# Kernel tuning notes

Measured on AMD Instinct MI355X. Metric: run time of the kernel, lower is better.

Reference implementation:

```python
import jax, jax.numpy as jnp
import numpy as np

TOP_K = 2
NORM_TOPK_PROB = True


def setup_inputs() -> dict:
    key = jax.random.key(0)
    k1, k2 = jax.random.split(key)
    hidden_states = jax.random.normal(k1, (4, 4096, 2048), dtype=jnp.float32)
    # gate weight [n_routed_experts, hidden_size], kaiming-uniform-like scale
    weight = jax.random.normal(k2, (64, 2048), dtype=jnp.float32) * 0.02
    return {"hidden_states": hidden_states, "weight": weight}


def reference(hidden_states, weight):
    bsz, seq_len, h = hidden_states.shape
    x = hidden_states.reshape(-1, h)                      # [T, H]
    logits = jnp.einsum("th,eh->te", x, weight)           # [T, E]
    scores = jax.nn.softmax(logits, axis=-1)              # [T, E]
    topk_weight, topk_idx = jax.lax.top_k(scores, TOP_K)  # [T, K] each
    if TOP_K > 1 and NORM_TOPK_PROB:
        topk_weight = topk_weight / (topk_weight.sum(axis=-1, keepdims=True) + 1e-20)
    return (topk_idx.reshape(bsz, seq_len, -1), topk_weight.reshape(bsz, seq_len, -1))
```

## Files before the change

kernel.cpp:

```cpp
#include <hip/hip_runtime.h>
#include <math.h>

#define H    2048
#define NE   64
#define TOKB 32
#define KC   64
#define NCH  (H / KC)
#define TAU  4.0e-3f
#define NEGF (-3.0e38f)

typedef __bf16 bf16x8 __attribute__((ext_vector_type(8)));
typedef float  f32x16 __attribute__((ext_vector_type(16)));

#define MFMA(a, b, c) __builtin_amdgcn_mfma_f32_32x32x16_bf16((a), (b), (c), 0, 0, 0)
#define LD4(p) (*reinterpret_cast<const float4*>(p))

__device__ __forceinline__ void cvt8(const float4 a, const float4 b,
                                     bf16x8& hi, bf16x8& lo) {
    const float v0 = a.x, v1 = a.y, v2 = a.z, v3 = a.w;
    const float v4 = b.x, v5 = b.y, v6 = b.z, v7 = b.w;
    hi[0] = (__bf16)v0; lo[0] = (__bf16)(v0 - (float)hi[0]);
    hi[1] = (__bf16)v1; lo[1] = (__bf16)(v1 - (float)hi[1]);
    hi[2] = (__bf16)v2; lo[2] = (__bf16)(v2 - (float)hi[2]);
    hi[3] = (__bf16)v3; lo[3] = (__bf16)(v3 - (float)hi[3]);
    hi[4] = (__bf16)v4; lo[4] = (__bf16)(v4 - (float)hi[4]);
    hi[5] = (__bf16)v5; lo[5] = (__bf16)(v5 - (float)hi[5]);
    hi[6] = (__bf16)v6; lo[6] = (__bf16)(v6 - (float)hi[6]);
    hi[7] = (__bf16)v7; lo[7] = (__bf16)(v7 - (float)hi[7]);
}

__device__ __forceinline__ void gll16(const float* g, float* l) {
    __builtin_amdgcn_global_load_lds(
        (const __attribute__((address_space(1))) void*)g,
        (__attribute__((address_space(3))) void*)l, 16, 0, 0);
}

__global__ void zero_wl(int* __restrict__ wl) {
    if (threadIdx.x == 0) wl[0] = 0;
}

__global__ __launch_bounds__(256) void moe_gate_mfma(
    const float* __restrict__ x,
    const float* __restrict__ w,
    float* __restrict__ out,
    int woff,
    int* __restrict__ wl, int wlcap)
{
    __shared__ float lds[2][6144];

    const int tid  = threadIdx.x;
    const int lane = tid & 63;
    const int kq   = tid >> 6;
    const int lo5  = lane & 31;
    const int hi5  = lane >> 5;
    const int t0   = blockIdx.x * TOKB;

    const float* sbase[6];
    #pragma unroll
    for (int s = 0; s < 6; ++s) {
        const int idx = kq * 1536 + s * 256 + lane * 4;
        const int tr  = (idx & 4095) >> 6;
        const int sl  = (lane & 15) ^ (tr & 15);
        sbase[s] = (idx < 4096)
            ? (w + (size_t)tr * H + sl * 4)
            : (x + (size_t)(t0 + tr) * H + sl * 4);
    }

    f32x16 acc0, acc1;
    #pragma unroll
    for (int i = 0; i < 16; ++i) { acc0[i] = 0.f; acc1[i] = 0.f; }

    #pragma unroll
    for (int s = 0; s < 6; ++s)
        gll16(sbase[s], &lds[0][kq * 1536 + s * 256]);
    __syncthreads();

    const int s0 = kq * 4 + hi5 * 2;

    for (int c = 0; c < NCH; ++c) {
        const int cur = c & 1;
        if (c + 1 < NCH) {
            const int kc = (c + 1) * KC;
            #pragma unroll
            for (int s = 0; s < 6; ++s)
                gll16(sbase[s] + kc, &lds[cur ^ 1][kq * 1536 + s * 256]);
        }

        const float* buf = lds[cur];
        const int rb  = lo5;
        const int ra0 = lo5, ra1 = 32 + lo5;

        const float4 b1  = LD4(&buf[4096 + rb * 64 + ((s0     ^ (rb  & 15)) << 2)]);
        const float4 b2  = LD4(&buf[4096 + rb * 64 + (((s0+1) ^ (rb  & 15)) << 2)]);
        const float4 a01 = LD4(&buf[       ra0 * 64 + ((s0     ^ (ra0 & 15)) << 2)]);
        const float4 a02 = LD4(&buf[       ra0 * 64 + (((s0+1) ^ (ra0 & 15)) << 2)]);
        const float4 a11 = LD4(&buf[       ra1 * 64 + ((s0     ^ (ra1 & 15)) << 2)]);
        const float4 a12 = LD4(&buf[       ra1 * 64 + (((s0+1) ^ (ra1 & 15)) << 2)]);

        bf16x8 bh, bl, ah0, al0, ah1, al1;
        cvt8(b1, b2, bh, bl);
        cvt8(a01, a02, ah0, al0);
        cvt8(a11, a12, ah1, al1);

        acc0 = MFMA(ah0, bh, acc0);
        acc1 = MFMA(ah1, bh, acc1);
        acc0 = MFMA(ah0, bl, acc0);
        acc1 = MFMA(ah1, bl, acc1);
        acc0 = MFMA(al0, bh, acc0);
        acc1 = MFMA(al1, bh, acc1);

        __syncthreads();
    }

    float* S = &lds[0][0];
    if (kq != 0) {
        const int base = ((kq - 1) * 32 + lo5) * 65;
        #pragma unroll
        for (int r = 0; r < 16; ++r) {
            const int e0 = (r & 3) + 8 * (r >> 2) + 4 * hi5;
            S[base + e0]      = acc0[r];
            S[base + 32 + e0] = acc1[r];
        }
    }
    __syncthreads();
    if (kq != 0) return;
    #pragma unroll
    for (int q = 0; q < 3; ++q) {
        const int base = (q * 32 + lo5) * 65;
        #pragma unroll
        for (int r = 0; r < 16; ++r) {
            const int e0 = (r & 3) + 8 * (r >> 2) + 4 * hi5;
            acc0[r] += S[base + e0];
            acc1[r] += S[base + 32 + e0];
        }
    }

    float m1 = NEGF, m2 = NEGF, m3 = NEGF;
    int   i1 = 0, i2 = 0;
    #pragma unroll
    for (int r = 0; r < 16; ++r) {
        const float v = acc0[r];
        const int   e = (r & 3) + 8 * (r >> 2) + 4 * hi5;
        if (v > m1)      { m3 = m2; m2 = m1; i2 = i1; m1 = v; i1 = e; }
        else if (v > m2) { m3 = m2; m2 = v; i2 = e; }
        else if (v > m3) { m3 = v; }
    }
    #pragma unroll
    for (int r = 0; r < 16; ++r) {
        const float v = acc1[r];
        const int   e = 32 + (r & 3) + 8 * (r >> 2) + 4 * hi5;
        if (v > m1)      { m3 = m2; m2 = m1; i2 = i1; m1 = v; i1 = e; }
        else if (v > m2) { m3 = m2; m2 = v; i2 = e; }
        else if (v > m3) { m3 = v; }
    }

    const float n1 = __shfl_xor(m1, 32), n2 = __shfl_xor(m2, 32), n3 = __shfl_xor(m3, 32);
    const int   j1 = __shfl_xor(i1, 32), j2 = __shfl_xor(i2, 32);

    float a1, a2, a3, b1, b2, b3; int ia1, ia2, ib1, ib2;
    const bool aF = (m1 > n1) || (m1 == n1 && i1 < j1);
    if (aF) { a1=m1; a2=m2; a3=m3; ia1=i1; ia2=i2; b1=n1; b2=n2; b3=n3; ib1=j1; ib2=j2; }
    else    { a1=n1; a2=n2; a3=n3; ia1=j1; ia2=j2; b1=m1; b2=m2; b3=m3; ib1=i1; ib2=i2; }

    const float o1 = a1; const int oi1 = ia1;
    float o2, o3; int oi2;
    const bool a2F = (a2 > b1) || (a2 == b1 && ia2 < ib1);
    if (a2F) { o2 = a2; oi2 = ia2; o3 = (a3 > b1) ? a3 : b1; }
    else     { o2 = b1; oi2 = ib1; o3 = (a2 > b2) ? a2 : b2; }

    if (hi5 == 0) {
        const int t = t0 + lo5;
        const float r = expf(o2 - o1);
        const float s = 1.0f + r;
        out[2 * t + 0]        = (float)oi1;
        out[2 * t + 1]        = (float)oi2;
        out[woff + 2 * t + 0] = 1.0f / s;
        out[woff + 2 * t + 1] = r / s;
        if ((o1 - o2 < TAU) || (o2 - o3 < TAU)) {
            const int pos = atomicAdd(wl, 1);
            if (pos < wlcap) wl[1 + pos] = t;
        }
    }
}

__global__ __launch_bounds__(256) void moe_refine_fp64(
    const float* __restrict__ x, const float* __restrict__ w,
    float* __restrict__ out, int woff,
    const int* __restrict__ wl, int wlcap)
{
    __shared__ double Sd[3][NE];
    const int lane = threadIdx.x & 63;
    const int wv   = threadIdx.x >> 6;
    const int ks   = wv * 512;
    int cnt = wl[0];
    if (cnt > wlcap) cnt = wlcap;

    for (int i = blockIdx.x; i < cnt; i += gridDim.x) {
        const int t = wl[1 + i];

        const float4 xa = LD4(&x[(size_t)t * H + ks + lane * 4]);
        const float4 xb = LD4(&x[(size_t)t * H + ks + 256 + lane * 4]);
        const double x0 = xa.x, x1 = xa.y, x2 = xa.z, x3 = xa.w;
        const double x4 = xb.x, x5 = xb.y, x6 = xb.z, x7 = xb.w;

        double myacc = 0.0;
        #pragma unroll 4
        for (int e = 0; e < NE; ++e) {
            const float4 wa = LD4(&w[(size_t)e * H + ks + lane * 4]);
            const float4 wb = LD4(&w[(size_t)e * H + ks + 256 + lane * 4]);
            double sA = 0.0, sB = 0.0;
            sA = fma((double)wa.x, x0, sA); sA = fma((double)wa.y, x1, sA);
            sA = fma((double)wa.z, x2, sA); sA = fma((double)wa.w, x3, sA);
            sB = fma((double)wb.x, x4, sB); sB = fma((double)wb.y, x5, sB);
            sB = fma((double)wb.z, x6, sB); sB = fma((double)wb.w, x7, sB);
            double s = sA + sB;
            #pragma unroll
            for (int off = 1; off < 64; off <<= 1)
                s += __shfl_xor(s, off);
            if (lane == e) myacc = s;
        }

        if (wv > 0) Sd[wv - 1][lane] = myacc;
        __syncthreads();
        if (wv == 0) {
            const double acc = ((myacc + Sd[0][lane]) + Sd[1][lane]) + Sd[2][lane];

            double v = acc; int bi = lane;
            #pragma unroll
            for (int off = 32; off > 0; off >>= 1) {
                double ov = __shfl_xor(v, off);
                int    oi = __shfl_xor(bi, off);
                if (ov > v || (ov == v && oi < bi)) { v = ov; bi = oi; }
            }
            const double m1 = v; const int i1 = bi;

            double v2 = (lane == i1) ? -1.0e300 : acc; int b2 = lane;
            #pragma unroll
            for (int off = 32; off > 0; off >>= 1) {
                double ov = __shfl_xor(v2, off);
                int    oi = __shfl_xor(b2, off);
                if (ov > v2 || (ov == v2 && oi < b2)) { v2 = ov; b2 = oi; }
            }
            const double m2 = v2; const int i2 = b2;

            if (lane == 0) {
                const double r = exp(m2 - m1);
                const double s = 1.0 + r;
                out[2 * t + 0]        = (float)i1;
                out[2 * t + 1]        = (float)i2;
                out[woff + 2 * t + 0] = (float)(1.0 / s);
                out[woff + 2 * t + 1] = (float)(r / s);
            }
        }
        __syncthreads();
    }
}

extern "C" void kernel_launch(void* const* d_in, const int* in_sizes, int n_in,
                              void* d_out, int out_size, void* d_ws, size_t ws_size,
                              hipStream_t stream) {
    const float* x   = (const float*)d_in[0];
    const float* wgt = (const float*)d_in[1];
    float* out = (float*)d_out;

    const int T    = in_sizes[0] / H;
    const int woff = out_size / 2;

    int* wl = (int*)d_ws;
    int wlcap = (int)(ws_size / sizeof(int)) - 1;
    if (wlcap > T) wlcap = T;

    zero_wl<<<dim3(1), dim3(64), 0, stream>>>(wl);

    moe_gate_mfma<<<dim3(T / TOKB), dim3(256), 0, stream>>>(
        x, wgt, out, woff, wl, wlcap);

    moe_refine_fp64<<<dim3(512), dim3(256), 0, stream>>>(
        x, wgt, out, woff, wl, wlcap);
}
```

Before: 74.56 us.

## Double token tile, triple-buffer LDS with waitcnt-based pipelining

Each block now handles 64 tokens instead of 32, using four waves arranged as two token tiles by two K halves. The K chunk is halved so each stage fits a three-buffer LDS ring, and global-to-LDS loads are issued two chunks ahead. The per-chunk __syncthreads is replaced by an explicit vmcnt wait plus a barrier. This is meant to halve weight reloads per token and hide load latency better, at the cost of a shorter K-reduction per wave, fewer blocks, and correctness that depends on the hand-set vmcnt count.

```diff
diff --git a/kernel.cpp b/kernel.cpp
--- a/kernel.cpp
+++ b/kernel.cpp
@@ -3,9 +3,10 @@
 
 #define H    2048
 #define NE   64
-#define TOKB 32
-#define KC   64
+#define TOKB 64
+#define KC   32
 #define NCH  (H / KC)
+#define NBUF 3
 #define TAU  4.0e-3f
 #define NEGF (-3.0e38f)
 
@@ -46,22 +47,24 @@
     int woff,
     int* __restrict__ wl, int wlcap)
 {
-    __shared__ float lds[2][6144];
+    __shared__ float lds[NBUF][4096];
 
     const int tid  = threadIdx.x;
     const int lane = tid & 63;
-    const int kq   = tid >> 6;
+    const int wv   = tid >> 6;
+    const int mt   = wv >> 1;
+    const int kh   = wv & 1;
     const int lo5  = lane & 31;
     const int hi5  = lane >> 5;
     const int t0   = blockIdx.x * TOKB;
 
-    const float* sbase[6];
-    #pragma unroll
-    for (int s = 0; s < 6; ++s) {
-        const int idx = kq * 1536 + s * 256 + lane * 4;
-        const int tr  = (idx & 4095) >> 6;
-        const int sl  = (lane & 15) ^ (tr & 15);
-        sbase[s] = (idx < 4096)
+    const float* sbase[4];
+    #pragma unroll
+    for (int s = 0; s < 4; ++s) {
+        const int idx = (wv * 4 + s) * 256 + lane * 4;
+        const int tr  = (idx & 2047) >> 5;
+        const int sl  = ((idx >> 2) & 7) ^ (tr & 7);
+        sbase[s] = (idx < 2048)
             ? (w + (size_t)tr * H + sl * 4)
             : (x + (size_t)(t0 + tr) * H + sl * 4);
     }
@@ -71,31 +74,35 @@
     for (int i = 0; i < 16; ++i) { acc0[i] = 0.f; acc1[i] = 0.f; }
 
     #pragma unroll
-    for (int s = 0; s < 6; ++s)
-        gll16(sbase[s], &lds[0][kq * 1536 + s * 256]);
-    __syncthreads();
-
-    const int s0 = kq * 4 + hi5 * 2;
-
+    for (int s = 0; s < 4; ++s) gll16(sbase[s],      &lds[0][(wv * 4 + s) * 256]);
+    #pragma unroll
+    for (int s = 0; s < 4; ++s) gll16(sbase[s] + KC, &lds[1][(wv * 4 + s) * 256]);
+
+    const int s0  = kh * 4 + hi5 * 2;
+    const int xk  = lo5 & 7;
+    const int rb  = mt * 32 + lo5;
+    const int ra0 = lo5, ra1 = 32 + lo5;
+    const int obB  = 2048 + rb * 32;
+    const int obA0 = ra0 * 32, obA1 = ra1 * 32;
+    const int c0 = ((s0)     ^ xk) << 2;
+    const int c1 = ((s0 + 1) ^ xk) << 2;
+
+    int ib = 0, iw = 2;
     for (int c = 0; c < NCH; ++c) {
-        const int cur = c & 1;
-        if (c + 1 < NCH) {
-            const int kc = (c + 1) * KC;
-            #pragma unroll
-            for (int s = 0; s < 6; ++s)
-                gll16(sbase[s] + kc, &lds[cur ^ 1][kq * 1536 + s * 256]);
-        }
-
-        const float* buf = lds[cur];
-        const int rb  = lo5;
-        const int ra0 = lo5, ra1 = 32 + lo5;
-
-        const float4 b1  = LD4(&buf[4096 + rb * 64 + ((s0     ^ (rb  & 15)) << 2)]);
-        const float4 b2  = LD4(&buf[4096 + rb * 64 + (((s0+1) ^ (rb  & 15)) << 2)]);
-        const float4 a01 = LD4(&buf[       ra0 * 64 + ((s0     ^ (ra0 & 15)) << 2)]);
-        const float4 a02 = LD4(&buf[       ra0 * 64 + (((s0+1) ^ (ra0 & 15)) << 2)]);
-        const float4 a11 = LD4(&buf[       ra1 * 64 + ((s0     ^ (ra1 & 15)) << 2)]);
-        const float4 a12 = LD4(&buf[       ra1 * 64 + (((s0+1) ^ (ra1 & 15)) << 2)]);
+        if (c < NCH - 1) {
+            asm volatile("s_waitcnt vmcnt(4)" ::: "memory");
+        } else {
+            asm volatile("s_waitcnt vmcnt(0)" ::: "memory");
+        }
+        __builtin_amdgcn_s_barrier();
+
+        const float* buf = lds[ib];
+        const float4 b1  = LD4(&buf[obB  + c0]);
+        const float4 b2  = LD4(&buf[obB  + c1]);
+        const float4 a01 = LD4(&buf[obA0 + c0]);
+        const float4 a02 = LD4(&buf[obA0 + c1]);
+        const float4 a11 = LD4(&buf[obA1 + c0]);
+        const float4 a12 = LD4(&buf[obA1 + c1]);
 
         bf16x8 bh, bl, ah0, al0, ah1, al1;
         cvt8(b1, b2, bh, bl);
@@ -109,12 +116,20 @@
         acc0 = MFMA(al0, bh, acc0);
         acc1 = MFMA(al1, bh, acc1);
 
-        __syncthreads();
-    }
-
+        if (c + 2 < NCH) {
+            const int kc = (c + 2) * KC;
+            #pragma unroll
+            for (int s = 0; s < 4; ++s)
+                gll16(sbase[s] + kc, &lds[iw][(wv * 4 + s) * 256]);
+        }
+        ib = (ib == NBUF - 1) ? 0 : ib + 1;
+        iw = (iw == NBUF - 1) ? 0 : iw + 1;
+    }
+
+    __syncthreads();
     float* S = &lds[0][0];
-    if (kq != 0) {
-        const int base = ((kq - 1) * 32 + lo5) * 65;
+    if (kh == 1) {
+        const int base = (mt * 32 + lo5) * 65;
         #pragma unroll
         for (int r = 0; r < 16; ++r) {
             const int e0 = (r & 3) + 8 * (r >> 2) + 4 * hi5;
@@ -123,10 +138,9 @@
         }
     }
     __syncthreads();
-    if (kq != 0) return;
-    #pragma unroll
-    for (int q = 0; q < 3; ++q) {
-        const int base = (q * 32 + lo5) * 65;
+    if (kh == 1) return;
+    {
+        const int base = (mt * 32 + lo5) * 65;
         #pragma unroll
         for (int r = 0; r < 16; ++r) {
             const int e0 = (r & 3) + 8 * (r >> 2) + 4 * hi5;
@@ -169,7 +183,7 @@
     else     { o2 = b1; oi2 = ib1; o3 = (a2 > b2) ? a2 : b2; }
 
     if (hi5 == 0) {
-        const int t = t0 + lo5;
+        const int t = t0 + mt * 32 + lo5;
         const float r = expf(o2 - o1);
         const float s = 1.0f + r;
         out[2 * t + 0]        = (float)oi1;
```

New measurement: 64.66 us. 13.3% less time.
